# Performance work log

Measured on AMD Instinct MI355X. Metric: run time of the kernel, lower is better.

Reference implementation:

```python
import jax, jax.numpy as jnp
import numpy as np

N = 100000      # nodes
E = 3200000     # edges
G = 256         # graphs in batch
EPS = 1e-5      # BatchNorm eps


def gcn_conv(x, W, b, src, dst, norm):
    # x: [N, Fin] -> [N, Fout]. PyG GCNConv: linear, then sym-normalized
    # scatter-add over edges (self-loops already included in src/dst/norm).
    h = x @ W                                   # [N, Fout]
    msg = h[src] * norm[:, None]                # [E+N, Fout] gather + scale
    out = jax.ops.segment_sum(msg, dst, num_segments=N)
    return out + b


def bn_eval(x, gamma, beta, rm, rv):
    return (x - rm) * jax.lax.rsqrt(rv + EPS) * gamma + beta


def setup_inputs() -> dict:
    key = jax.random.key(0)
    ks = jax.random.split(key, 24)
    x = jax.random.normal(ks[0], (N, 8), dtype=jnp.float32)
    edge_index = jax.random.randint(ks[1], (2, E), 0, N, dtype=jnp.int64)
    batch = jnp.sort(jax.random.randint(ks[2], (N,), 0, G, dtype=jnp.int64))

    def lin(k, fin, fout):
        return jax.random.normal(k, (fin, fout), dtype=jnp.float32) / np.sqrt(fin)

    d = {
        "x": x, "edge_index": edge_index, "batch": batch,
        "W1": lin(ks[3], 8, 64),  "b1": jnp.zeros((64,), jnp.float32),
        "g1": jnp.ones((64,), jnp.float32), "be1": jnp.zeros((64,), jnp.float32),
        "rm1": jax.random.normal(ks[4], (64,), jnp.float32) * 0.1,
        "rv1": jnp.ones((64,), jnp.float32) + jax.random.uniform(ks[5], (64,)) * 0.1,
        "W2": lin(ks[6], 64, 64), "b2": jnp.zeros((64,), jnp.float32),
        "g2": jnp.ones((64,), jnp.float32), "be2": jnp.zeros((64,), jnp.float32),
        "rm2": jax.random.normal(ks[7], (64,), jnp.float32) * 0.1,
        "rv2": jnp.ones((64,), jnp.float32) + jax.random.uniform(ks[8], (64,)) * 0.1,
        "W3": lin(ks[9], 64, 64), "b3": jnp.zeros((64,), jnp.float32),
        "g3": jnp.ones((64,), jnp.float32), "be3": jnp.zeros((64,), jnp.float32),
        "rm3": jax.random.normal(ks[10], (64,), jnp.float32) * 0.1,
        "rv3": jnp.ones((64,), jnp.float32) + jax.random.uniform(ks[11], (64,)) * 0.1,
        "Wr1": lin(ks[12], 64, 64), "br1": jnp.zeros((64,), jnp.float32),
        "Wr2": lin(ks[13], 64, 2),  "br2": jnp.zeros((2,), jnp.float32),
    }
    return d


def reference(x, edge_index, batch,
              W1, b1, g1, be1, rm1, rv1,
              W2, b2, g2, be2, rm2, rv2,
              W3, b3, g3, be3, rm3, rv3,
              Wr1, br1, Wr2, br2):
    # add self-loops once; compute symmetric normalization deg^-1/2
    loops = jnp.arange(N, dtype=edge_index.dtype)
    src = jnp.concatenate([edge_index[0], loops])   # [E+N]
    dst = jnp.concatenate([edge_index[1], loops])
    deg = jax.ops.segment_sum(jnp.ones_like(dst, dtype=x.dtype), dst, num_segments=N)
    dinv = jnp.where(deg > 0, jax.lax.rsqrt(deg), 0.0)
    norm = dinv[src] * dinv[dst]                    # [E+N]

    h = jax.nn.relu(bn_eval(gcn_conv(x, W1, b1, src, dst, norm), g1, be1, rm1, rv1))
    h = jax.nn.relu(bn_eval(gcn_conv(h, W2, b2, src, dst, norm), g2, be2, rm2, rv2))
    h = jax.nn.relu(bn_eval(gcn_conv(h, W3, b3, src, dst, norm), g3, be3, rm3, rv3))

    # global mean pool over graph ids
    sums = jax.ops.segment_sum(h, batch, num_segments=G)           # [G, 64]
    cnts = jax.ops.segment_sum(jnp.ones((N,), h.dtype), batch, num_segments=G)
    pooled = sums / jnp.maximum(cnts, 1.0)[:, None]

    out = jax.nn.relu(pooled @ Wr1 + br1) @ Wr2 + br2              # [G, 2]
    return out
```

## Files before the change

### kernel.cpp

```cpp
#include <hip/hip_runtime.h>
#include <hip/hip_fp16.h>

#define NN 100000
#define NE 3200000
#define NG 256
#define NF (NN * 64)
#define FEPS 1e-5f
#define BSH 8
#define NB ((NN + 255) >> 8)
#define CHA 8192

static inline int ceil_div(int a, int b) { return (a + b - 1) / b; }


__global__ __launch_bounds__(256) void kA_hist(const int* __restrict__ dst,
                                               int* __restrict__ bh) {
    __shared__ int lh[NB];
    int t = threadIdx.x;
    for (int b = t; b < NB; b += 256) lh[b] = 0;
    __syncthreads();
    int e0 = blockIdx.x * CHA;
    int e1 = min(e0 + CHA, NE);
    for (int i = e0 + t; i < e1; i += 256) atomicAdd(&lh[dst[i] >> BSH], 1);
    __syncthreads();
    for (int b = t; b < NB; b += 256)
        if (lh[b]) atomicAdd(&bh[b], lh[b]);
}

__global__ __launch_bounds__(512) void kA_scan(const int* __restrict__ bh,
                                               int* __restrict__ bboff,
                                               int* __restrict__ bcur) {
    __shared__ int s[512];
    int t = threadIdx.x;
    int v = (t < NB) ? bh[t] : 0;
    s[t] = v;
    __syncthreads();
    for (int off = 1; off < 512; off <<= 1) {
        int add = (t >= off) ? s[t - off] : 0;
        __syncthreads();
        s[t] += add;
        __syncthreads();
    }
    if (t < NB) {
        int ex = s[t] - v;
        bboff[t] = ex;
        bcur[t] = ex;
    }
    if (t == 0) bboff[NB] = NE;
}

__global__ __launch_bounds__(256) void kA_fill(const int* __restrict__ src,
                                               const int* __restrict__ dst,
                                               int* __restrict__ bcur,
                                               int2* __restrict__ ebuf) {
    __shared__ int lh[NB];
    __shared__ int lbase[NB];
    __shared__ int lcur[NB];
    int t = threadIdx.x;
    for (int b = t; b < NB; b += 256) lh[b] = 0;
    __syncthreads();
    int e0 = blockIdx.x * CHA;
    int e1 = min(e0 + CHA, NE);
    for (int i = e0 + t; i < e1; i += 256) atomicAdd(&lh[dst[i] >> BSH], 1);
    __syncthreads();
    for (int b = t; b < NB; b += 256) {
        int c = lh[b];
        lbase[b] = c ? atomicAdd(&bcur[b], c) : 0;
        lcur[b] = 0;
    }
    __syncthreads();
    for (int i = e0 + t; i < e1; i += 256) {
        int d = dst[i];
        int s = src[i];
        int b = d >> BSH;
        int p = atomicAdd(&lcur[b], 1);
        ebuf[lbase[b] + p] = make_int2(s, d);
    }
}


__global__ __launch_bounds__(256) void kB_hist(const int2* __restrict__ ebuf,
                                               const int* __restrict__ bboff,
                                               int* __restrict__ cnt) {
    __shared__ int lc[256];
    int b = blockIdx.x;
    int t = threadIdx.x;
    lc[t] = 0;
    __syncthreads();
    int st = bboff[b], en = bboff[b + 1];
    for (int i = st + t; i < en; i += 256) atomicAdd(&lc[ebuf[i].y & 255], 1);
    __syncthreads();
    int node = (b << BSH) + t;
    if (node < NN) cnt[node] = lc[t];
}

__global__ __launch_bounds__(256) void k_dinv_xs(const int* __restrict__ cnt,
                                                 const float* __restrict__ x,
                                                 float* __restrict__ dinv,
                                                 __half* __restrict__ xs) {
    int i = blockIdx.x * 256 + threadIdx.x;
    if (i >= NN) return;
    float di = rsqrtf((float)cnt[i] + 1.0f);
    dinv[i] = di;
#pragma unroll
    for (int f = 0; f < 8; ++f) xs[i * 8 + f] = __float2half(x[i * 8 + f] * di);
}

__global__ __launch_bounds__(256) void k_scan1(const int* __restrict__ cnt,
                                               int* __restrict__ bsum) {
    __shared__ int s[256];
    int t = threadIdx.x;
    int i = blockIdx.x * 256 + t;
    s[t] = (i < NN) ? cnt[i] : 0;
    __syncthreads();
    for (int off = 128; off > 0; off >>= 1) {
        if (t < off) s[t] += s[t + off];
        __syncthreads();
    }
    if (t == 0) bsum[blockIdx.x] = s[0];
}

__global__ __launch_bounds__(512) void k_scan2(int* __restrict__ bsum, int nb) {
    __shared__ int s[512];
    int t = threadIdx.x;
    int v = (t < nb) ? bsum[t] : 0;
    s[t] = v;
    __syncthreads();
    for (int off = 1; off < 512; off <<= 1) {
        int add = (t >= off) ? s[t - off] : 0;
        __syncthreads();
        s[t] += add;
        __syncthreads();
    }
    if (t < nb) bsum[t] = s[t] - v;
}

__global__ __launch_bounds__(256) void k_scan3(const int* __restrict__ cnt,
                                               const int* __restrict__ bsum,
                                               int* __restrict__ rowptr) {
    __shared__ int s[256];
    int t = threadIdx.x;
    int i = blockIdx.x * 256 + t;
    int v = (i < NN) ? cnt[i] : 0;
    s[t] = v;
    __syncthreads();
    for (int off = 1; off < 256; off <<= 1) {
        int add = (t >= off) ? s[t - off] : 0;
        __syncthreads();
        s[t] += add;
        __syncthreads();
    }
    if (i < NN) rowptr[i] = s[t] - v + bsum[blockIdx.x];
}

__global__ __launch_bounds__(256) void kB_fill(const int2* __restrict__ ebuf,
                                               const int* __restrict__ bboff,
                                               const int* __restrict__ rowptr,
                                               int* __restrict__ csr) {
    __shared__ int rp[256];
    __shared__ int lc[256];
    int b = blockIdx.x;
    int t = threadIdx.x;
    int node = (b << BSH) + t;
    rp[t] = (node < NN) ? rowptr[node] : 0;
    lc[t] = 0;
    __syncthreads();
    int st = bboff[b], en = bboff[b + 1];
    for (int i = st + t; i < en; i += 256) {
        int2 e = ebuf[i];
        int dl = e.y & 255;
        int p = atomicAdd(&lc[dl], 1);
        csr[rp[dl] + p] = e.x;
    }
}

__global__ __launch_bounds__(256) void k_cnts(const int* __restrict__ batch,
                                              float* __restrict__ cnts) {
    int c = blockIdx.x * 256 + threadIdx.x;
    int n0 = c * 64;
    if (n0 >= NN) return;
    int n1 = min(n0 + 64, NN);
    int gcur = batch[n0];
    float cf = 0.f;
    for (int n = n0; n < n1; ++n) {
        int gg = batch[n];
        if (gg != gcur) {
            atomicAdd(&cnts[gcur], cf);
            cf = 0.f;
            gcur = gg;
        }
        cf += 1.f;
    }
    atomicAdd(&cnts[gcur], cf);
}


__global__ __launch_bounds__(256) void k_gxf8(const __half2* __restrict__ xs2,
                                              const int* __restrict__ rowptr,
                                              const int* __restrict__ cnt,
                                              const float* __restrict__ dinv,
                                              const int* __restrict__ csr,
                                              const float* __restrict__ W,
                                              const float* __restrict__ b,
                                              const float* __restrict__ g,
                                              const float* __restrict__ be,
                                              const float* __restrict__ rm,
                                              const float* __restrict__ rv,
                                              __half* __restrict__ out) {
    __shared__ float Ws[512];
    int tid = threadIdx.x;
    for (int i = tid; i < 512; i += 256) Ws[i] = W[i];
    __syncthreads();
    int wave = (blockIdx.x * 256 + tid) >> 6;
    int lane = tid & 63;
    if (wave >= NN) return;
    int es = lane >> 2, q = lane & 3;
    int st = rowptr[wave], n = cnt[wave];
    float ax = 0.f, ay = 0.f;
    for (int k0 = 0; k0 < n; k0 += 16) {
        int kk = k0 + es;
        if (kk < n) {
            float2 f = __half22float2(xs2[csr[st + kk] * 4 + q]);
            ax += f.x; ay += f.y;
        }
    }
    ax += __shfl_xor(ax, 4, 64);  ay += __shfl_xor(ay, 4, 64);
    ax += __shfl_xor(ax, 8, 64);  ay += __shfl_xor(ay, 8, 64);
    ax += __shfl_xor(ax, 16, 64); ay += __shfl_xor(ay, 16, 64);
    ax += __shfl_xor(ax, 32, 64); ay += __shfl_xor(ay, 32, 64);
    float di = dinv[wave];
    float2 s2 = __half22float2(xs2[wave * 4 + q]);
    float pfx = (ax + s2.x) * di;
    float pfy = (ay + s2.y) * di;
    float scale = g[lane] * rsqrtf(rv[lane] + FEPS);
    float shift = be[lane] + (b[lane] - rm[lane]) * scale;
    float o = 0.f;
#pragma unroll
    for (int qq = 0; qq < 4; ++qq) {
        float vx = __shfl(pfx, qq, 64);
        float vy = __shfl(pfy, qq, 64);
        o = fmaf(vx, Ws[(2 * qq) * 64 + lane], o);
        o = fmaf(vy, Ws[(2 * qq + 1) * 64 + lane], o);
    }
    o = fmaxf(fmaf(o, scale, shift), 0.f);
    out[wave * 64 + lane] = __float2half(o * di);
}

template <bool POOL>
__global__ __launch_bounds__(256) void k_gxf64(const __half2* __restrict__ Hin2,
                                               const int* __restrict__ rowptr,
                                               const int* __restrict__ cnt,
                                               const float* __restrict__ dinv,
                                               const int* __restrict__ csr,
                                               const float* __restrict__ W,
                                               const float* __restrict__ b,
                                               const float* __restrict__ g,
                                               const float* __restrict__ be,
                                               const float* __restrict__ rm,
                                               const float* __restrict__ rv,
                                               const int* __restrict__ batch,
                                               __half* __restrict__ out,
                                               float* __restrict__ sums) {
    __shared__ float Ws[4096];
    int tid = threadIdx.x;
    for (int i = tid; i < 4096; i += 256) Ws[i] = W[i];
    __syncthreads();
    int wave = (blockIdx.x * 256 + tid) >> 6;
    int lane = tid & 63;
    if (wave >= NN) return;
    int p = lane >> 5;
    int q = lane & 31;
    int st = rowptr[wave], n = cnt[wave];
    float ax = 0.f, ay = 0.f;
    int k = 0;
    while (k < n) {
        int rem = n - k;
        int chunk = rem < 64 ? rem : 64;
        int eidx = (lane < chunk) ? csr[st + k + lane] : 0;
        int j = 0;
        for (; j + 16 <= chunk; j += 16) {
            int s0 = __shfl(eidx, j + 0 + p, 64);
            int s1 = __shfl(eidx, j + 2 + p, 64);
            int s2 = __shfl(eidx, j + 4 + p, 64);
            int s3 = __shfl(eidx, j + 6 + p, 64);
            int s4 = __shfl(eidx, j + 8 + p, 64);
            int s5 = __shfl(eidx, j + 10 + p, 64);
            int s6 = __shfl(eidx, j + 12 + p, 64);
            int s7 = __shfl(eidx, j + 14 + p, 64);
            float2 f0 = __half22float2(Hin2[s0 * 32 + q]);
            float2 f1 = __half22float2(Hin2[s1 * 32 + q]);
            float2 f2 = __half22float2(Hin2[s2 * 32 + q]);
            float2 f3 = __half22float2(Hin2[s3 * 32 + q]);
            float2 f4 = __half22float2(Hin2[s4 * 32 + q]);
            float2 f5 = __half22float2(Hin2[s5 * 32 + q]);
            float2 f6 = __half22float2(Hin2[s6 * 32 + q]);
            float2 f7 = __half22float2(Hin2[s7 * 32 + q]);
            ax += ((f0.x + f1.x) + (f2.x + f3.x)) + ((f4.x + f5.x) + (f6.x + f7.x));
            ay += ((f0.y + f1.y) + (f2.y + f3.y)) + ((f4.y + f5.y) + (f6.y + f7.y));
        }
        for (; j + 2 <= chunk; j += 2) {
            int s = __shfl(eidx, j + p, 64);
            float2 f = __half22float2(Hin2[s * 32 + q]);
            ax += f.x; ay += f.y;
        }
        if (j < chunk) {
            int s = __shfl(eidx, j, 64);
            if (p == 0) {
                float2 f = __half22float2(Hin2[s * 32 + q]);
                ax += f.x; ay += f.y;
            }
        }
        k += chunk;
    }
    ax += __shfl_xor(ax, 32, 64);
    ay += __shfl_xor(ay, 32, 64);
    float di = dinv[wave];
    float2 s2 = __half22float2(Hin2[wave * 32 + q]);
    float pfx = (ax + s2.x) * di;
    float pfy = (ay + s2.y) * di;
    float scale = g[lane] * rsqrtf(rv[lane] + FEPS);
    float shift = be[lane] + (b[lane] - rm[lane]) * scale;
    float o0 = 0.f, o1 = 0.f;
#pragma unroll
    for (int qq = 0; qq < 32; ++qq) {
        float vx = __shfl(pfx, qq, 64);
        float vy = __shfl(pfy, qq, 64);
        o0 = fmaf(vx, Ws[(2 * qq) * 64 + lane], o0);
        o1 = fmaf(vy, Ws[(2 * qq + 1) * 64 + lane], o1);
    }
    float o = o0 + o1;
    o = fmaxf(fmaf(o, scale, shift), 0.f);
    if (POOL) {
        int gg = batch[wave];
        atomicAdd(&sums[gg * 64 + lane], o);
    } else {
        out[wave * 64 + lane] = __float2half(o * di);
    }
}


__global__ __launch_bounds__(256) void k_head(const float* __restrict__ sums,
                                              const float* __restrict__ cnts,
                                              const float* __restrict__ Wr1,
                                              const float* __restrict__ br1,
                                              const float* __restrict__ Wr2,
                                              const float* __restrict__ br2,
                                              float* __restrict__ out) {
    int wave = (blockIdx.x * 256 + threadIdx.x) >> 6;
    int lane = threadIdx.x & 63;
    if (wave >= NG) return;
    float c = fmaxf(cnts[wave], 1.0f);
    float pooled = sums[wave * 64 + lane] / c;
    float acc = 0.f;
#pragma unroll
    for (int k = 0; k < 64; ++k)
        acc = fmaf(__shfl(pooled, k, 64), Wr1[k * 64 + lane], acc);
    float hid = fmaxf(acc + br1[lane], 0.f);
    float o0 = hid * Wr2[lane * 2 + 0];
    float o1 = hid * Wr2[lane * 2 + 1];
#pragma unroll
    for (int off = 32; off > 0; off >>= 1) {
        o0 += __shfl_xor(o0, off, 64);
        o1 += __shfl_xor(o1, off, 64);
    }
    if (lane == 0) {
        out[wave * 2 + 0] = o0 + br2[0];
        out[wave * 2 + 1] = o1 + br2[1];
    }
}

extern "C" void kernel_launch(void* const* d_in, const int* in_sizes, int n_in,
                              void* d_out, int out_size, void* d_ws, size_t ws_size,
                              hipStream_t stream) {
    const float* x   = (const float*)d_in[0];
    const int*   ei  = (const int*)d_in[1];
    const int*   bat = (const int*)d_in[2];
    const float* W1  = (const float*)d_in[3];
    const float* b1  = (const float*)d_in[4];
    const float* g1  = (const float*)d_in[5];
    const float* be1 = (const float*)d_in[6];
    const float* rm1 = (const float*)d_in[7];
    const float* rv1 = (const float*)d_in[8];
    const float* W2  = (const float*)d_in[9];
    const float* b2  = (const float*)d_in[10];
    const float* g2  = (const float*)d_in[11];
    const float* be2 = (const float*)d_in[12];
    const float* rm2 = (const float*)d_in[13];
    const float* rv2 = (const float*)d_in[14];
    const float* W3  = (const float*)d_in[15];
    const float* b3  = (const float*)d_in[16];
    const float* g3  = (const float*)d_in[17];
    const float* be3 = (const float*)d_in[18];
    const float* rm3 = (const float*)d_in[19];
    const float* rv3 = (const float*)d_in[20];
    const float* Wr1 = (const float*)d_in[21];
    const float* br1 = (const float*)d_in[22];
    const float* Wr2 = (const float*)d_in[23];
    const float* br2 = (const float*)d_in[24];
    float* out = (float*)d_out;

    int*    cnt    = (int*)d_ws;
    int*    rowptr = cnt + NN;
    int*    bsum   = rowptr + NN;
    int*    bh     = bsum + 512;
    int*    bboff  = bh + NB;
    int*    bcur   = bboff + NB + 1;
    float*  dinv   = (float*)(bcur + NB);
    int*    csr    = (int*)(dinv + NN);
    __half* xs     = (__half*)(csr + NE);
    float*  sums   = (float*)(xs + NN * 8);
    float*  cnts   = sums + NG * 64;
    __half* A      = (__half*)(cnts + NG);
    __half* B      = A + NF;
    int2*   ebuf   = (int2*)A;

    const int* srcI = ei;
    const int* dstI = ei + NE;

    const int gA = ceil_div(NE, CHA);
    const int gN = ceil_div(NN, 256);
    const int gW = ceil_div(NN * 64, 256);

    hipMemsetAsync(bh, 0, NB * sizeof(int), stream);
    hipMemsetAsync(sums, 0, (NG * 64 + NG) * sizeof(float), stream);

    kA_hist<<<gA, 256, 0, stream>>>(dstI, bh);
    kA_scan<<<1, 512, 0, stream>>>(bh, bboff, bcur);
    kA_fill<<<gA, 256, 0, stream>>>(srcI, dstI, bcur, ebuf);

    kB_hist<<<NB, 256, 0, stream>>>(ebuf, bboff, cnt);
    k_dinv_xs<<<gN, 256, 0, stream>>>(cnt, x, dinv, xs);
    k_cnts<<<ceil_div(ceil_div(NN, 64), 256), 256, 0, stream>>>(bat, cnts);
    k_scan1<<<gN, 256, 0, stream>>>(cnt, bsum);
    k_scan2<<<1, 512, 0, stream>>>(bsum, gN);
    k_scan3<<<gN, 256, 0, stream>>>(cnt, bsum, rowptr);
    kB_fill<<<NB, 256, 0, stream>>>(ebuf, bboff, rowptr, csr);

    k_gxf8<<<gW, 256, 0, stream>>>((const __half2*)xs, rowptr, cnt, dinv, csr,
                                   W1, b1, g1, be1, rm1, rv1, A);
    k_gxf64<false><<<gW, 256, 0, stream>>>((const __half2*)A, rowptr, cnt, dinv, csr,
                                           W2, b2, g2, be2, rm2, rv2,
                                           bat, B, nullptr);
    k_gxf64<true><<<gW, 256, 0, stream>>>((const __half2*)B, rowptr, cnt, dinv, csr,
                                          W3, b3, g3, be3, rm3, rv3,
                                          bat, nullptr, sums);

    k_head<<<ceil_div(NG * 64, 256), 256, 0, stream>>>(sums, cnts, Wr1, br1, Wr2, br2, out);
}
```

Before: 619.8 us.

## Partition CSR neighbors by source-range and aggregate in cache-sized phases

Builds a CSR whose per-destination neighbor lists are sub-sorted into five source-node ranges, fusing the histogram, scan and fill steps into one per-bucket kernel and dropping the three global scan kernels. Each 64-wide GCN layer is then split into five launches, each gathering only neighbors from one source range, so the gathered feature slice (about 2.5 MB of fp16) can stay resident in cache. Partial sums go to an fp32 accumulator buffer, which costs extra global traffic and launches. The gather inner unroll is also reduced from 16 to 8.

```diff
diff --git a/kernel.cpp b/kernel.cpp
--- a/kernel.cpp
+++ b/kernel.cpp
@@ -9,6 +9,8 @@
 #define BSH 8
 #define NB ((NN + 255) >> 8)
 #define CHA 8192
+#define NCB 5
+#define SRCB 20000
 
 static inline int ceil_div(int a, int b) { return (a + b - 1) / b; }
 
@@ -29,7 +31,8 @@
 
 __global__ __launch_bounds__(512) void kA_scan(const int* __restrict__ bh,
                                                int* __restrict__ bboff,
-                                               int* __restrict__ bcur) {
+                                               int* __restrict__ bcur,
+                                               int* __restrict__ rowptr2) {
     __shared__ int s[512];
     int t = threadIdx.x;
     int v = (t < NB) ? bh[t] : 0;
@@ -46,7 +49,10 @@
         bboff[t] = ex;
         bcur[t] = ex;
     }
-    if (t == 0) bboff[NB] = NE;
+    if (t == 0) {
+        bboff[NB] = NE;
+        rowptr2[NN * NCB] = NE;
+    }
 }
 
 __global__ __launch_bounds__(256) void kA_fill(const int* __restrict__ src,
@@ -78,20 +84,55 @@
     }
 }
 
-
-__global__ __launch_bounds__(256) void kB_hist(const int2* __restrict__ ebuf,
-                                               const int* __restrict__ bboff,
-                                               int* __restrict__ cnt) {
-    __shared__ int lc[256];
-    int b = blockIdx.x;
-    int t = threadIdx.x;
-    lc[t] = 0;
+__global__ __launch_bounds__(256) void kB(const int2* __restrict__ ebuf,
+                                          const int* __restrict__ bboff,
+                                          int* __restrict__ rowptr2,
+                                          int* __restrict__ csr,
+                                          int* __restrict__ cnt) {
+    __shared__ int h[256 * NCB];
+    __shared__ int s[256];
+    int b = blockIdx.x, t = threadIdx.x;
+    for (int i = t; i < 256 * NCB; i += 256) h[i] = 0;
     __syncthreads();
     int st = bboff[b], en = bboff[b + 1];
-    for (int i = st + t; i < en; i += 256) atomicAdd(&lc[ebuf[i].y & 255], 1);
-    __syncthreads();
+    for (int i = st + t; i < en; i += 256) {
+        int2 e = ebuf[i];
+        int cb = e.x / SRCB;
+        atomicAdd(&h[(e.y & 255) * NCB + cb], 1);
+    }
+    __syncthreads();
+    int c0 = h[t * NCB + 0], c1 = h[t * NCB + 1], c2 = h[t * NCB + 2];
+    int c3 = h[t * NCB + 3], c4 = h[t * NCB + 4];
+    int tot = c0 + c1 + c2 + c3 + c4;
+    s[t] = tot;
+    __syncthreads();
+    for (int off = 1; off < 256; off <<= 1) {
+        int add = (t >= off) ? s[t - off] : 0;
+        __syncthreads();
+        s[t] += add;
+        __syncthreads();
+    }
+    int ex = s[t] - tot;
+    int base = bboff[b];
+    int o0 = ex, o1 = o0 + c0, o2 = o1 + c1, o3 = o2 + c2, o4 = o3 + c3;
+    h[t * NCB + 0] = o0; h[t * NCB + 1] = o1; h[t * NCB + 2] = o2;
+    h[t * NCB + 3] = o3; h[t * NCB + 4] = o4;
     int node = (b << BSH) + t;
-    if (node < NN) cnt[node] = lc[t];
+    if (node < NN) {
+        cnt[node] = tot;
+        rowptr2[node * NCB + 0] = base + o0;
+        rowptr2[node * NCB + 1] = base + o1;
+        rowptr2[node * NCB + 2] = base + o2;
+        rowptr2[node * NCB + 3] = base + o3;
+        rowptr2[node * NCB + 4] = base + o4;
+    }
+    __syncthreads();
+    for (int i = st + t; i < en; i += 256) {
+        int2 e = ebuf[i];
+        int cb = e.x / SRCB;
+        int pos = atomicAdd(&h[(e.y & 255) * NCB + cb], 1);
+        csr[base + pos] = e.x;
+    }
 }
 
 __global__ __launch_bounds__(256) void k_dinv_xs(const int* __restrict__ cnt,
@@ -104,74 +145,6 @@
     dinv[i] = di;
 #pragma unroll
     for (int f = 0; f < 8; ++f) xs[i * 8 + f] = __float2half(x[i * 8 + f] * di);
-}
-
-__global__ __launch_bounds__(256) void k_scan1(const int* __restrict__ cnt,
-                                               int* __restrict__ bsum) {
-    __shared__ int s[256];
-    int t = threadIdx.x;
-    int i = blockIdx.x * 256 + t;
-    s[t] = (i < NN) ? cnt[i] : 0;
-    __syncthreads();
-    for (int off = 128; off > 0; off >>= 1) {
-        if (t < off) s[t] += s[t + off];
-        __syncthreads();
-    }
-    if (t == 0) bsum[blockIdx.x] = s[0];
-}
-
-__global__ __launch_bounds__(512) void k_scan2(int* __restrict__ bsum, int nb) {
-    __shared__ int s[512];
-    int t = threadIdx.x;
-    int v = (t < nb) ? bsum[t] : 0;
-    s[t] = v;
-    __syncthreads();
-    for (int off = 1; off < 512; off <<= 1) {
-        int add = (t >= off) ? s[t - off] : 0;
-        __syncthreads();
-        s[t] += add;
-        __syncthreads();
-    }
-    if (t < nb) bsum[t] = s[t] - v;
-}
-
-__global__ __launch_bounds__(256) void k_scan3(const int* __restrict__ cnt,
-                                               const int* __restrict__ bsum,
-                                               int* __restrict__ rowptr) {
-    __shared__ int s[256];
-    int t = threadIdx.x;
-    int i = blockIdx.x * 256 + t;
-    int v = (i < NN) ? cnt[i] : 0;
-    s[t] = v;
-    __syncthreads();
-    for (int off = 1; off < 256; off <<= 1) {
-        int add = (t >= off) ? s[t - off] : 0;
-        __syncthreads();
-        s[t] += add;
-        __syncthreads();
-    }
-    if (i < NN) rowptr[i] = s[t] - v + bsum[blockIdx.x];
-}
-
-__global__ __launch_bounds__(256) void kB_fill(const int2* __restrict__ ebuf,
-                                               const int* __restrict__ bboff,
-                                               const int* __restrict__ rowptr,
-                                               int* __restrict__ csr) {
-    __shared__ int rp[256];
-    __shared__ int lc[256];
-    int b = blockIdx.x;
-    int t = threadIdx.x;
-    int node = (b << BSH) + t;
-    rp[t] = (node < NN) ? rowptr[node] : 0;
-    lc[t] = 0;
-    __syncthreads();
-    int st = bboff[b], en = bboff[b + 1];
-    for (int i = st + t; i < en; i += 256) {
-        int2 e = ebuf[i];
-        int dl = e.y & 255;
-        int p = atomicAdd(&lc[dl], 1);
-        csr[rp[dl] + p] = e.x;
-    }
 }
 
 __global__ __launch_bounds__(256) void k_cnts(const int* __restrict__ batch,
@@ -196,8 +169,7 @@
 
 
 __global__ __launch_bounds__(256) void k_gxf8(const __half2* __restrict__ xs2,
-                                              const int* __restrict__ rowptr,
-                                              const int* __restrict__ cnt,
+                                              const int* __restrict__ rowptr2,
                                               const float* __restrict__ dinv,
                                               const int* __restrict__ csr,
                                               const float* __restrict__ W,
@@ -215,7 +187,8 @@
     int lane = tid & 63;
     if (wave >= NN) return;
     int es = lane >> 2, q = lane & 3;
-    int st = rowptr[wave], n = cnt[wave];
+    int st = rowptr2[wave * NCB];
+    int n = rowptr2[wave * NCB + NCB] - st;
     float ax = 0.f, ay = 0.f;
     for (int k0 = 0; k0 < n; k0 += 16) {
         int kk = k0 + es;
@@ -246,14 +219,15 @@
     out[wave * 64 + lane] = __float2half(o * di);
 }
 
-template <bool POOL>
-__global__ __launch_bounds__(256) void k_gxf64(const __half2* __restrict__ Hin2,
-                                               const int* __restrict__ rowptr,
-                                               const int* __restrict__ cnt,
+template <int PH>
+__global__ __launch_bounds__(256) void k_phase(const __half2* __restrict__ Hin2,
+                                               const int* __restrict__ rowptr2,
+                                               int cb0,
                                                const float* __restrict__ dinv,
                                                const int* __restrict__ csr,
+                                               float* __restrict__ acc,
                                                const float* __restrict__ W,
-                                               const float* __restrict__ b,
+                                               const float* __restrict__ bb,
                                                const float* __restrict__ g,
                                                const float* __restrict__ be,
                                                const float* __restrict__ rm,
@@ -261,16 +235,19 @@
                                                const int* __restrict__ batch,
                                                __half* __restrict__ out,
                                                float* __restrict__ sums) {
-    __shared__ float Ws[4096];
+    __shared__ float Ws[(PH >= 2) ? 4096 : 1];
     int tid = threadIdx.x;
-    for (int i = tid; i < 4096; i += 256) Ws[i] = W[i];
-    __syncthreads();
+    if (PH >= 2) {
+        for (int i = tid; i < 4096; i += 256) Ws[i] = W[i];
+        __syncthreads();
+    }
     int wave = (blockIdx.x * 256 + tid) >> 6;
     int lane = tid & 63;
     if (wave >= NN) return;
     int p = lane >> 5;
     int q = lane & 31;
-    int st = rowptr[wave], n = cnt[wave];
+    int st = rowptr2[wave * NCB + cb0];
+    int n = rowptr2[wave * NCB + cb0 + 1] - st;
     float ax = 0.f, ay = 0.f;
     int k = 0;
     while (k < n) {
@@ -278,25 +255,17 @@
         int chunk = rem < 64 ? rem : 64;
         int eidx = (lane < chunk) ? csr[st + k + lane] : 0;
         int j = 0;
-        for (; j + 16 <= chunk; j += 16) {
+        for (; j + 8 <= chunk; j += 8) {
             int s0 = __shfl(eidx, j + 0 + p, 64);
             int s1 = __shfl(eidx, j + 2 + p, 64);
             int s2 = __shfl(eidx, j + 4 + p, 64);
             int s3 = __shfl(eidx, j + 6 + p, 64);
-            int s4 = __shfl(eidx, j + 8 + p, 64);
-            int s5 = __shfl(eidx, j + 10 + p, 64);
-            int s6 = __shfl(eidx, j + 12 + p, 64);
-            int s7 = __shfl(eidx, j + 14 + p, 64);
             float2 f0 = __half22float2(Hin2[s0 * 32 + q]);
             float2 f1 = __half22float2(Hin2[s1 * 32 + q]);
             float2 f2 = __half22float2(Hin2[s2 * 32 + q]);
             float2 f3 = __half22float2(Hin2[s3 * 32 + q]);
-            float2 f4 = __half22float2(Hin2[s4 * 32 + q]);
-            float2 f5 = __half22float2(Hin2[s5 * 32 + q]);
-            float2 f6 = __half22float2(Hin2[s6 * 32 + q]);
-            float2 f7 = __half22float2(Hin2[s7 * 32 + q]);
-            ax += ((f0.x + f1.x) + (f2.x + f3.x)) + ((f4.x + f5.x) + (f6.x + f7.x));
-            ay += ((f0.y + f1.y) + (f2.y + f3.y)) + ((f4.y + f5.y) + (f6.y + f7.y));
+            ax += (f0.x + f1.x) + (f2.x + f3.x);
+            ay += (f0.y + f1.y) + (f2.y + f3.y);
         }
         for (; j + 2 <= chunk; j += 2) {
             int s = __shfl(eidx, j + p, 64);
@@ -314,27 +283,32 @@
     }
     ax += __shfl_xor(ax, 32, 64);
     ay += __shfl_xor(ay, 32, 64);
-    float di = dinv[wave];
-    float2 s2 = __half22float2(Hin2[wave * 32 + q]);
-    float pfx = (ax + s2.x) * di;
-    float pfy = (ay + s2.y) * di;
-    float scale = g[lane] * rsqrtf(rv[lane] + FEPS);
-    float shift = be[lane] + (b[lane] - rm[lane]) * scale;
-    float o0 = 0.f, o1 = 0.f;
+    float v = p ? ay : ax;
+    int aoff = wave * 64 + 2 * q + p;
+    if (PH == 0) {
+        float sf = __half2float(((const __half*)Hin2)[aoff]);
+        acc[aoff] = v + sf;
+    } else if (PH == 1) {
+        acc[aoff] += v;
+    } else {
+        float di = dinv[wave];
+        float pf = (acc[aoff] + v) * di;
+        float scale = g[lane] * rsqrtf(rv[lane] + FEPS);
+        float shift = be[lane] + (bb[lane] - rm[lane]) * scale;
+        float o0 = 0.f, o1 = 0.f;
 #pragma unroll
-    for (int qq = 0; qq < 32; ++qq) {
-        float vx = __shfl(pfx, qq, 64);
-        float vy = __shfl(pfy, qq, 64);
-        o0 = fmaf(vx, Ws[(2 * qq) * 64 + lane], o0);
-        o1 = fmaf(vy, Ws[(2 * qq + 1) * 64 + lane], o1);
-    }
-    float o = o0 + o1;
-    o = fmaxf(fmaf(o, scale, shift), 0.f);
-    if (POOL) {
-        int gg = batch[wave];
-        atomicAdd(&sums[gg * 64 + lane], o);
-    } else {
-        out[wave * 64 + lane] = __float2half(o * di);
+        for (int f = 0; f < 64; f += 2) {
+            float va = __shfl(pf, (f >> 1), 64);
+            float vb = __shfl(pf, 32 + (f >> 1), 64);
+            o0 = fmaf(va, Ws[f * 64 + lane], o0);
+            o1 = fmaf(vb, Ws[(f + 1) * 64 + lane], o1);
+        }
+        float o = fmaxf(fmaf(o0 + o1, scale, shift), 0.f);
+        if (PH == 2) {
+            out[wave * 64 + lane] = __float2half(o * di);
+        } else {
+            atomicAdd(&sums[batch[wave] * 64 + lane], o);
+        }
     }
 }
 
@@ -399,20 +373,20 @@
     const float* br2 = (const float*)d_in[24];
     float* out = (float*)d_out;
 
-    int*    cnt    = (int*)d_ws;
-    int*    rowptr = cnt + NN;
-    int*    bsum   = rowptr + NN;
-    int*    bh     = bsum + 512;
-    int*    bboff  = bh + NB;
-    int*    bcur   = bboff + NB + 1;
-    float*  dinv   = (float*)(bcur + NB);
-    int*    csr    = (int*)(dinv + NN);
-    __half* xs     = (__half*)(csr + NE);
-    float*  sums   = (float*)(xs + NN * 8);
-    float*  cnts   = sums + NG * 64;
-    __half* A      = (__half*)(cnts + NG);
-    __half* B      = A + NF;
-    int2*   ebuf   = (int2*)A;
+    int*    cnt     = (int*)d_ws;
+    int*    rowptr2 = cnt + NN;
+    int*    bh      = rowptr2 + NN * NCB + 1;
+    int*    bboff   = bh + NB;
+    int*    bcur    = bboff + NB + 1;
+    float*  dinv    = (float*)(bcur + NB);
+    int*    csr     = (int*)(dinv + NN);
+    __half* xs      = (__half*)(csr + NE);
+    float*  sums    = (float*)(xs + NN * 8);
+    float*  cnts    = sums + NG * 64;
+    __half* A       = (__half*)(cnts + NG);
+    __half* B       = A + NF;
+    float*  acc     = (float*)(B + NF);
+    int2*   ebuf    = (int2*)acc;
 
     const int* srcI = ei;
     const int* dstI = ei + NE;
@@ -425,25 +399,36 @@
     hipMemsetAsync(sums, 0, (NG * 64 + NG) * sizeof(float), stream);
 
     kA_hist<<<gA, 256, 0, stream>>>(dstI, bh);
-    kA_scan<<<1, 512, 0, stream>>>(bh, bboff, bcur);
+    kA_scan<<<1, 512, 0, stream>>>(bh, bboff, bcur, rowptr2);
     kA_fill<<<gA, 256, 0, stream>>>(srcI, dstI, bcur, ebuf);
-
-    kB_hist<<<NB, 256, 0, stream>>>(ebuf, bboff, cnt);
+    kB<<<NB, 256, 0, stream>>>(ebuf, bboff, rowptr2, csr, cnt);
     k_dinv_xs<<<gN, 256, 0, stream>>>(cnt, x, dinv, xs);
     k_cnts<<<ceil_div(ceil_div(NN, 64), 256), 256, 0, stream>>>(bat, cnts);
-    k_scan1<<<gN, 256, 0, stream>>>(cnt, bsum);
-    k_scan2<<<1, 512, 0, stream>>>(bsum, gN);
-    k_scan3<<<gN, 256, 0, stream>>>(cnt, bsum, rowptr);
-    kB_fill<<<NB, 256, 0, stream>>>(ebuf, bboff, rowptr, csr);
-
-    k_gxf8<<<gW, 256, 0, stream>>>((const __half2*)xs, rowptr, cnt, dinv, csr,
+
+    k_gxf8<<<gW, 256, 0, stream>>>((const __half2*)xs, rowptr2, dinv, csr,
                                    W1, b1, g1, be1, rm1, rv1, A);
-    k_gxf64<false><<<gW, 256, 0, stream>>>((const __half2*)A, rowptr, cnt, dinv, csr,
-                                           W2, b2, g2, be2, rm2, rv2,
-                                           bat, B, nullptr);
-    k_gxf64<true><<<gW, 256, 0, stream>>>((const __half2*)B, rowptr, cnt, dinv, csr,
-                                          W3, b3, g3, be3, rm3, rv3,
-                                          bat, nullptr, sums);
+
+    k_phase<0><<<gW, 256, 0, stream>>>((const __half2*)A, rowptr2, 0, dinv, csr, acc,
+                                       W2, b2, g2, be2, rm2, rv2, bat, B, sums);
+    k_phase<1><<<gW, 256, 0, stream>>>((const __half2*)A, rowptr2, 1, dinv, csr, acc,
+                                       W2, b2, g2, be2, rm2, rv2, bat, B, sums);
+    k_phase<1><<<gW, 256, 0, stream>>>((const __half2*)A, rowptr2, 2, dinv, csr, acc,
+                                       W2, b2, g2, be2, rm2, rv2, bat, B, sums);
+    k_phase<1><<<gW, 256, 0, stream>>>((const __half2*)A, rowptr2, 3, dinv, csr, acc,
+                                       W2, b2, g2, be2, rm2, rv2, bat, B, sums);
+    k_phase<2><<<gW, 256, 0, stream>>>((const __half2*)A, rowptr2, 4, dinv, csr, acc,
+                                       W2, b2, g2, be2, rm2, rv2, bat, B, sums);
+
+    k_phase<0><<<gW, 256, 0, stream>>>((const __half2*)B, rowptr2, 0, dinv, csr, acc,
+                                       W3, b3, g3, be3, rm3, rv3, bat, A, sums);
+    k_phase<1><<<gW, 256, 0, stream>>>((const __half2*)B, rowptr2, 1, dinv, csr, acc,
+                                       W3, b3, g3, be3, rm3, rv3, bat, A, sums);
+    k_phase<1><<<gW, 256, 0, stream>>>((const __half2*)B, rowptr2, 2, dinv, csr, acc,
+                                       W3, b3, g3, be3, rm3, rv3, bat, A, sums);
+    k_phase<1><<<gW, 256, 0, stream>>>((const __half2*)B, rowptr2, 3, dinv, csr, acc,
+                                       W3, b3, g3, be3, rm3, rv3, bat, A, sums);
+    k_phase<3><<<gW, 256, 0, stream>>>((const __half2*)B, rowptr2, 4, dinv, csr, acc,
+                                       W3, b3, g3, be3, rm3, rv3, bat, A, sums);
 
     k_head<<<ceil_div(NG * 64, 256), 256, 0, stream>>>(sums, cnts, Wr1, br1, Wr2, br2, out);
 }
```

Result: slower. 807.8 us (+30.3%).

## Split layer-2 aggregation into four feature-block passes for cache-resident gathers

Applied to the files above, without the earlier changes.

Layer 1 now writes its output in a feature-blocked layout (four 16-feature slabs of 3.2 MB each). Layer 2's gather runs as four separate passes, one per slab, so each pass's random gather footprint is small enough to stay cache-resident. A separate transform kernel then applies W2, BN and ReLU. Layer 3 uses a new per-lane 64-wide gather kernel with 8-way unrolled loads. The cost is extra launches and an fp32 partial-sum buffer that is written and re-read, plus four re-reads of the CSR indices.

```diff
diff --git a/kernel.cpp b/kernel.cpp
--- a/kernel.cpp
+++ b/kernel.cpp
@@ -206,7 +206,7 @@
                                               const float* __restrict__ be,
                                               const float* __restrict__ rm,
                                               const float* __restrict__ rv,
-                                              __half* __restrict__ out) {
+                                              __half* __restrict__ Afb) {
     __shared__ float Ws[512];
     int tid = threadIdx.x;
     for (int i = tid; i < 512; i += 256) Ws[i] = W[i];
@@ -214,13 +214,13 @@
     int wave = (blockIdx.x * 256 + tid) >> 6;
     int lane = tid & 63;
     if (wave >= NN) return;
-    int es = lane >> 2, q = lane & 3;
+    int es = lane >> 2, q4 = lane & 3;
     int st = rowptr[wave], n = cnt[wave];
     float ax = 0.f, ay = 0.f;
     for (int k0 = 0; k0 < n; k0 += 16) {
         int kk = k0 + es;
         if (kk < n) {
-            float2 f = __half22float2(xs2[csr[st + kk] * 4 + q]);
+            float2 f = __half22float2(xs2[csr[st + kk] * 4 + q4]);
             ax += f.x; ay += f.y;
         }
     }
@@ -229,7 +229,7 @@
     ax += __shfl_xor(ax, 16, 64); ay += __shfl_xor(ay, 16, 64);
     ax += __shfl_xor(ax, 32, 64); ay += __shfl_xor(ay, 32, 64);
     float di = dinv[wave];
-    float2 s2 = __half22float2(xs2[wave * 4 + q]);
+    float2 s2 = __half22float2(xs2[wave * 4 + q4]);
     float pfx = (ax + s2.x) * di;
     float pfy = (ay + s2.y) * di;
     float scale = g[lane] * rsqrtf(rv[lane] + FEPS);
@@ -243,99 +243,155 @@
         o = fmaf(vy, Ws[(2 * qq + 1) * 64 + lane], o);
     }
     o = fmaxf(fmaf(o, scale, shift), 0.f);
-    out[wave * 64 + lane] = __float2half(o * di);
-}
-
-template <bool POOL>
-__global__ __launch_bounds__(256) void k_gxf64(const __half2* __restrict__ Hin2,
-                                               const int* __restrict__ rowptr,
-                                               const int* __restrict__ cnt,
-                                               const float* __restrict__ dinv,
-                                               const int* __restrict__ csr,
-                                               const float* __restrict__ W,
-                                               const float* __restrict__ b,
-                                               const float* __restrict__ g,
-                                               const float* __restrict__ be,
-                                               const float* __restrict__ rm,
-                                               const float* __restrict__ rv,
-                                               const int* __restrict__ batch,
-                                               __half* __restrict__ out,
-                                               float* __restrict__ sums) {
-    __shared__ float Ws[4096];
+    int fb = lane >> 4;
+    Afb[(fb * NN + wave) * 16 + (lane & 15)] = __float2half(o * di);
+}
+
+__global__ __launch_bounds__(256) void k_pass(const __half2* __restrict__ Afb,
+                                              const int* __restrict__ rowptr,
+                                              const int* __restrict__ cnt,
+                                              const int* __restrict__ csr,
+                                              float2* __restrict__ P) {
     int tid = threadIdx.x;
-    for (int i = tid; i < 4096; i += 256) Ws[i] = W[i];
-    __syncthreads();
     int wave = (blockIdx.x * 256 + tid) >> 6;
     int lane = tid & 63;
     if (wave >= NN) return;
-    int p = lane >> 5;
-    int q = lane & 31;
+    int e3 = lane >> 3, q3 = lane & 7;
     int st = rowptr[wave], n = cnt[wave];
     float ax = 0.f, ay = 0.f;
     int k = 0;
     while (k < n) {
         int rem = n - k;
         int chunk = rem < 64 ? rem : 64;
-        int eidx = (lane < chunk) ? csr[st + k + lane] : 0;
-        int j = 0;
-        for (; j + 16 <= chunk; j += 16) {
-            int s0 = __shfl(eidx, j + 0 + p, 64);
-            int s1 = __shfl(eidx, j + 2 + p, 64);
-            int s2 = __shfl(eidx, j + 4 + p, 64);
-            int s3 = __shfl(eidx, j + 6 + p, 64);
-            int s4 = __shfl(eidx, j + 8 + p, 64);
-            int s5 = __shfl(eidx, j + 10 + p, 64);
-            int s6 = __shfl(eidx, j + 12 + p, 64);
-            int s7 = __shfl(eidx, j + 14 + p, 64);
-            float2 f0 = __half22float2(Hin2[s0 * 32 + q]);
-            float2 f1 = __half22float2(Hin2[s1 * 32 + q]);
-            float2 f2 = __half22float2(Hin2[s2 * 32 + q]);
-            float2 f3 = __half22float2(Hin2[s3 * 32 + q]);
-            float2 f4 = __half22float2(Hin2[s4 * 32 + q]);
-            float2 f5 = __half22float2(Hin2[s5 * 32 + q]);
-            float2 f6 = __half22float2(Hin2[s6 * 32 + q]);
-            float2 f7 = __half22float2(Hin2[s7 * 32 + q]);
-            ax += ((f0.x + f1.x) + (f2.x + f3.x)) + ((f4.x + f5.x) + (f6.x + f7.x));
-            ay += ((f0.y + f1.y) + (f2.y + f3.y)) + ((f4.y + f5.y) + (f6.y + f7.y));
-        }
-        for (; j + 2 <= chunk; j += 2) {
-            int s = __shfl(eidx, j + p, 64);
-            float2 f = __half22float2(Hin2[s * 32 + q]);
-            ax += f.x; ay += f.y;
-        }
-        if (j < chunk) {
-            int s = __shfl(eidx, j, 64);
-            if (p == 0) {
-                float2 f = __half22float2(Hin2[s * 32 + q]);
+        int ew = (lane < chunk) ? csr[st + k + lane] : 0;
+        if (chunk == 64) {
+#pragma unroll
+            for (int j = 0; j < 8; ++j) {
+                int s = __shfl(ew, j * 8 + e3, 64);
+                float2 f = __half22float2(Afb[s * 8 + q3]);
                 ax += f.x; ay += f.y;
+            }
+        } else {
+            for (int j = 0; j * 8 < chunk; ++j) {
+                int s = __shfl(ew, j * 8 + e3, 64);
+                if (j * 8 + e3 < chunk) {
+                    float2 f = __half22float2(Afb[s * 8 + q3]);
+                    ax += f.x; ay += f.y;
+                }
             }
         }
         k += chunk;
     }
-    ax += __shfl_xor(ax, 32, 64);
-    ay += __shfl_xor(ay, 32, 64);
-    float di = dinv[wave];
-    float2 s2 = __half22float2(Hin2[wave * 32 + q]);
-    float pfx = (ax + s2.x) * di;
-    float pfy = (ay + s2.y) * di;
+    ax += __shfl_xor(ax, 8, 64);  ay += __shfl_xor(ay, 8, 64);
+    ax += __shfl_xor(ax, 16, 64); ay += __shfl_xor(ay, 16, 64);
+    ax += __shfl_xor(ax, 32, 64); ay += __shfl_xor(ay, 32, 64);
+    if (e3 == 0) P[wave * 8 + q3] = make_float2(ax, ay);
+}
+
+__global__ __launch_bounds__(256) void k_xf2(const float* __restrict__ Pf,
+                                             const __half* __restrict__ Ah,
+                                             const float* __restrict__ dinv,
+                                             const float* __restrict__ W,
+                                             const float* __restrict__ bb,
+                                             const float* __restrict__ g,
+                                             const float* __restrict__ be,
+                                             const float* __restrict__ rm,
+                                             const float* __restrict__ rv,
+                                             __half* __restrict__ outRow) {
+    __shared__ float Ws[4096];
+    int tid = threadIdx.x;
+    for (int i = tid; i < 4096; i += 256) Ws[i] = W[i];
+    __syncthreads();
+    int wave = (blockIdx.x * 256 + tid) >> 6;
+    int lane = tid & 63;
+    if (wave >= NN) return;
+    int fb = lane >> 4, fl = lane & 15;
+    int idx = (fb * NN + wave) * 16 + fl;
+    float pf = (Pf[idx] + __half2float(Ah[idx])) * dinv[wave];
     float scale = g[lane] * rsqrtf(rv[lane] + FEPS);
-    float shift = be[lane] + (b[lane] - rm[lane]) * scale;
-    float o0 = 0.f, o1 = 0.f;
-#pragma unroll
-    for (int qq = 0; qq < 32; ++qq) {
-        float vx = __shfl(pfx, qq, 64);
-        float vy = __shfl(pfy, qq, 64);
-        o0 = fmaf(vx, Ws[(2 * qq) * 64 + lane], o0);
-        o1 = fmaf(vy, Ws[(2 * qq + 1) * 64 + lane], o1);
-    }
-    float o = o0 + o1;
+    float shift = be[lane] + (bb[lane] - rm[lane]) * scale;
+    float o0 = 0.f, o1 = 0.f, o2 = 0.f, o3 = 0.f;
+#pragma unroll
+    for (int k2 = 0; k2 < 64; k2 += 4) {
+        o0 = fmaf(__shfl(pf, k2 + 0, 64), Ws[(k2 + 0) * 64 + lane], o0);
+        o1 = fmaf(__shfl(pf, k2 + 1, 64), Ws[(k2 + 1) * 64 + lane], o1);
+        o2 = fmaf(__shfl(pf, k2 + 2, 64), Ws[(k2 + 2) * 64 + lane], o2);
+        o3 = fmaf(__shfl(pf, k2 + 3, 64), Ws[(k2 + 3) * 64 + lane], o3);
+    }
+    float o = (o0 + o1) + (o2 + o3);
     o = fmaxf(fmaf(o, scale, shift), 0.f);
-    if (POOL) {
-        int gg = batch[wave];
-        atomicAdd(&sums[gg * 64 + lane], o);
-    } else {
-        out[wave * 64 + lane] = __float2half(o * di);
-    }
+    outRow[wave * 64 + lane] = __float2half(o * dinv[wave]);
+}
+
+__global__ __launch_bounds__(256) void k_gx64p(const __half* __restrict__ Hin,
+                                               const int* __restrict__ rowptr,
+                                               const int* __restrict__ cnt,
+                                               const float* __restrict__ dinv,
+                                               const int* __restrict__ csr,
+                                               const float* __restrict__ W,
+                                               const float* __restrict__ bb,
+                                               const float* __restrict__ g,
+                                               const float* __restrict__ be,
+                                               const float* __restrict__ rm,
+                                               const float* __restrict__ rv,
+                                               const int* __restrict__ batch,
+                                               float* __restrict__ sums) {
+    __shared__ float Ws[4096];
+    int tid = threadIdx.x;
+    for (int i = tid; i < 4096; i += 256) Ws[i] = W[i];
+    __syncthreads();
+    int wave = (blockIdx.x * 256 + tid) >> 6;
+    int lane = tid & 63;
+    if (wave >= NN) return;
+    int st = rowptr[wave], n = cnt[wave];
+    float a0 = __half2float(Hin[wave * 64 + lane]);
+    float a1 = 0.f;
+    int k = 0;
+    while (k < n) {
+        int rem = n - k;
+        int chunk = rem < 64 ? rem : 64;
+        int ew = (lane < chunk) ? csr[st + k + lane] : 0;
+        int j = 0;
+        for (; j + 8 <= chunk; j += 8) {
+            int s0 = __shfl(ew, j + 0, 64);
+            int s1 = __shfl(ew, j + 1, 64);
+            int s2 = __shfl(ew, j + 2, 64);
+            int s3 = __shfl(ew, j + 3, 64);
+            int s4 = __shfl(ew, j + 4, 64);
+            int s5 = __shfl(ew, j + 5, 64);
+            int s6 = __shfl(ew, j + 6, 64);
+            int s7 = __shfl(ew, j + 7, 64);
+            float v0 = __half2float(Hin[s0 * 64 + lane]);
+            float v1 = __half2float(Hin[s1 * 64 + lane]);
+            float v2 = __half2float(Hin[s2 * 64 + lane]);
+            float v3 = __half2float(Hin[s3 * 64 + lane]);
+            float v4 = __half2float(Hin[s4 * 64 + lane]);
+            float v5 = __half2float(Hin[s5 * 64 + lane]);
+            float v6 = __half2float(Hin[s6 * 64 + lane]);
+            float v7 = __half2float(Hin[s7 * 64 + lane]);
+            a0 += (v0 + v1) + (v2 + v3);
+            a1 += (v4 + v5) + (v6 + v7);
+        }
+        for (; j < chunk; ++j) {
+            int s = __shfl(ew, j, 64);
+            a0 += __half2float(Hin[s * 64 + lane]);
+        }
+        k += chunk;
+    }
+    float pf = (a0 + a1) * dinv[wave];
+    float scale = g[lane] * rsqrtf(rv[lane] + FEPS);
+    float shift = be[lane] + (bb[lane] - rm[lane]) * scale;
+    float o0 = 0.f, o1 = 0.f, o2 = 0.f, o3 = 0.f;
+#pragma unroll
+    for (int k2 = 0; k2 < 64; k2 += 4) {
+        o0 = fmaf(__shfl(pf, k2 + 0, 64), Ws[(k2 + 0) * 64 + lane], o0);
+        o1 = fmaf(__shfl(pf, k2 + 1, 64), Ws[(k2 + 1) * 64 + lane], o1);
+        o2 = fmaf(__shfl(pf, k2 + 2, 64), Ws[(k2 + 2) * 64 + lane], o2);
+        o3 = fmaf(__shfl(pf, k2 + 3, 64), Ws[(k2 + 3) * 64 + lane], o3);
+    }
+    float o = (o0 + o1) + (o2 + o3);
+    o = fmaxf(fmaf(o, scale, shift), 0.f);
+    atomicAdd(&sums[batch[wave] * 64 + lane], o);
 }
 
 
@@ -410,9 +466,10 @@
     __half* xs     = (__half*)(csr + NE);
     float*  sums   = (float*)(xs + NN * 8);
     float*  cnts   = sums + NG * 64;
-    __half* A      = (__half*)(cnts + NG);
-    __half* B      = A + NF;
-    int2*   ebuf   = (int2*)A;
+    __half* Afb    = (__half*)(cnts + NG);
+    __half* B      = Afb + NF;
+    float*  P      = (float*)(B + NF);
+    int2*   ebuf   = (int2*)P;
 
     const int* srcI = ei;
     const int* dstI = ei + NE;
@@ -427,7 +484,6 @@
     kA_hist<<<gA, 256, 0, stream>>>(dstI, bh);
     kA_scan<<<1, 512, 0, stream>>>(bh, bboff, bcur);
     kA_fill<<<gA, 256, 0, stream>>>(srcI, dstI, bcur, ebuf);
-
     kB_hist<<<NB, 256, 0, stream>>>(ebuf, bboff, cnt);
     k_dinv_xs<<<gN, 256, 0, stream>>>(cnt, x, dinv, xs);
     k_cnts<<<ceil_div(ceil_div(NN, 64), 256), 256, 0, stream>>>(bat, cnts);
@@ -437,13 +493,18 @@
     kB_fill<<<NB, 256, 0, stream>>>(ebuf, bboff, rowptr, csr);
 
     k_gxf8<<<gW, 256, 0, stream>>>((const __half2*)xs, rowptr, cnt, dinv, csr,
-                                   W1, b1, g1, be1, rm1, rv1, A);
-    k_gxf64<false><<<gW, 256, 0, stream>>>((const __half2*)A, rowptr, cnt, dinv, csr,
-                                           W2, b2, g2, be2, rm2, rv2,
-                                           bat, B, nullptr);
-    k_gxf64<true><<<gW, 256, 0, stream>>>((const __half2*)B, rowptr, cnt, dinv, csr,
-                                          W3, b3, g3, be3, rm3, rv3,
-                                          bat, nullptr, sums);
+                                   W1, b1, g1, be1, rm1, rv1, Afb);
+
+    for (int fb = 0; fb < 4; ++fb) {
+        k_pass<<<gW, 256, 0, stream>>>((const __half2*)(Afb + fb * NN * 16),
+                                       rowptr, cnt, csr,
+                                       (float2*)(P + fb * NN * 16));
+    }
+    k_xf2<<<gW, 256, 0, stream>>>(P, Afb, dinv,
+                                  W2, b2, g2, be2, rm2, rv2, B);
+
+    k_gx64p<<<gW, 256, 0, stream>>>(B, rowptr, cnt, dinv, csr,
+                                    W3, b3, g3, be3, rm3, rv3, bat, sums);
 
     k_head<<<ceil_div(NG * 64, 256), 256, 0, stream>>>(sums, cnts, Wr1, br1, Wr2, br2, out);
 }
```

Result: slower. 754.7 us (+21.8%).
